# Kernel tuning notes

Hardware: AMD Instinct MI355X
Metric: run time of the kernel (lower is better)

Reference implementation:

```python
import jax, jax.numpy as jnp
import numpy as np

LEAKY_SLOPE = 0.01  # torch nn.LeakyReLU default

def leaky_relu(x):
    return jnp.where(x >= 0, x, LEAKY_SLOPE * x)

def setup_inputs() -> dict:
    key = jax.random.key(0)
    ks = jax.random.split(key, 11)
    B, F, C_IN, H, K, D = 2048, 512, 3, 64, 8, 128  # batch, features, expand, layer_conf[0], bucket_num, bucket_dim
    ASR, MM, OUT = 128, 768, 256
    proj_in = ASR + MM + F * D
    inp = {
        "stat_features": jax.random.uniform(ks[0], (B, F), dtype=jnp.float32),
        "asr_embeddings": jax.random.normal(ks[1], (B, ASR), dtype=jnp.float32),
        "mm_embeddings": jax.random.normal(ks[2], (B, MM), dtype=jnp.float32),
        "linear1_w": jax.random.normal(ks[3], (F, C_IN, H), dtype=jnp.float32) * (1.0 / np.sqrt(C_IN)),
        "linear1_b": jax.random.normal(ks[4], (F, 1, H), dtype=jnp.float32),
        "linear2_w": jax.random.normal(ks[5], (F, H, K), dtype=jnp.float32) * (1.0 / np.sqrt(H)),
        "linear2_b": jax.random.normal(ks[6], (F, 1, K), dtype=jnp.float32),
        "tau": jnp.ones((F, 1, K), dtype=jnp.float32),
        "emb": jax.random.normal(ks[7], (F, K, D), dtype=jnp.float32),
        "proj_w": jax.random.normal(ks[8], (OUT, proj_in), dtype=jnp.float32) * (1.0 / np.sqrt(proj_in)),
        "proj_b": jax.random.normal(ks[9], (OUT,), dtype=jnp.float32) * 0.01,
    }
    return inp

def reference(stat_features, asr_embeddings, mm_embeddings,
              linear1_w, linear1_b, linear2_w, linear2_b, tau, emb,
              proj_w, proj_b):
    # sanitize: NaN -> 0, negatives -> 0
    x = stat_features
    x = jnp.where(jnp.isnan(x) | (x < 0.0), 0.0, x)  # [B, F]

    # auto_dis: per-feature tiny MLP. x is expanded to 3 identical copies -> [B,F,1,3]
    # matmul with [F,3,H] == einsum over the 3 copies.
    B, F = x.shape
    x3 = jnp.broadcast_to(x[:, :, None], (B, F, 3))           # [B,F,3]
    h = jnp.einsum('bfc,fch->bfh', x3, linear1_w) + linear1_b[:, 0, :]  # [B,F,H]
    h = jnp.where(h >= 0, h, LEAKY_SLOPE * h)
    s = jnp.einsum('bfh,fhk->bfk', h, linear2_w) + linear2_b[:, 0, :]   # [B,F,K]
    s = jnp.where(s >= 0, s, LEAKY_SLOPE * s)
    s = s * tau[:, 0, :]
    p = jax.nn.softmax(s, axis=-1)                            # [B,F,K]
    y = jnp.einsum('bfk,fkd->bfd', p, emb)                    # [B,F,D]
    y = y.reshape(B, -1)                                      # [B, F*D] (fc = Identity)

    z = jnp.concatenate([asr_embeddings, mm_embeddings, y], axis=1)
    out = jax.nn.relu(z @ proj_w.T + proj_b)                  # [B, 256]
    return out
```

## Files before the change

### kernel.cpp

```cpp
#include <hip/hip_runtime.h>
#include <hip/hip_bf16.h>
#include <math.h>

#define LEAKY 0.01f
#define B_    2048
#define F_    512
#define H_    64
#define K_    8
#define D_    128
#define ASR_  128
#define MM_   768
#define OUT_  256
#define PROJ_IN 66432
#define ZK    4992
#define NSPLIT 4


typedef unsigned short u16;
typedef u16   u16x8 __attribute__((ext_vector_type(8)));
typedef short s16x8 __attribute__((ext_vector_type(8)));
typedef float f32x4 __attribute__((ext_vector_type(4)));

__device__ __forceinline__ u16 f2bf(float x) {
  unsigned int u = __float_as_uint(x);
  u += 0x7fffu + ((u >> 16) & 1u);
  return (u16)(u >> 16);
}

__device__ __forceinline__ float quad_sum(float g) {
  int a = __builtin_amdgcn_update_dpp(0, __float_as_int(g), 0xB1, 0xF, 0xF, true);
  g += __int_as_float(a);
  int b = __builtin_amdgcn_update_dpp(0, __float_as_int(g), 0x4E, 0xF, 0xF, true);
  return g + __int_as_float(b);
}

#define PRODUCER_BLOCKS (512 + 1024 + 896 + 224)

__global__ __launch_bounds__(256) void producer_kernel(
    const float* __restrict__ stat, const float* __restrict__ w1,
    const float* __restrict__ b1v, const float* __restrict__ w2,
    const float* __restrict__ b2v, const float* __restrict__ tauv,
    const float* __restrict__ pw, const float* __restrict__ emb,
    const float* __restrict__ asr, const float* __restrict__ mm,
    u16* __restrict__ A0, u16* __restrict__ Pf, u16* __restrict__ Wn) {
  __shared__ __align__(16) char smem[15616];
  const int bid = blockIdx.x;
  const int t = threadIdx.x;

  if (bid < 512) {
    const int f0 = (bid >> 3) * 8;
    const int o0 = (bid & 7) * 32;
    const int w = t >> 6, lam = t & 63;
    const int fl = lam >> 5, k = (lam >> 2) & 7, dq = lam & 3;
    const int fbase = f0 + 2 * w;
    float* sw = (float*)smem + w * 512;
    float* buf0 = sw;
    float* buf1 = sw + 256;
    const int wslot = lam ^ ((lam >> 3) & 7);
    const int xr = fl * 4 + dq;
    float4 e[8];
    {
      const float* ep = emb + ((size_t)(fbase + fl) * 8 + k) * 128 + dq * 32;
      #pragma unroll
      for (int j = 0; j < 8; ++j) e[j] = *(const float4*)(ep + j * 4);
    }
    const float* gsrc = pw + 896 + (size_t)fbase * 128
                        + (size_t)o0 * PROJ_IN + lam * 4;
    u16* wdst = Wn + (size_t)o0 * ZK + 896 + (size_t)(fbase + fl) * 8 + k;
    const float* rd0 = buf0 + fl * 128 + dq * 32;
    const float* rd1 = buf1 + fl * 128 + dq * 32;
    float4 va = *(const float4*)(gsrc);
    for (int rr = 0; rr < 16; ++rr) {
      const int r = 2 * rr;
      float4 vb = *(const float4*)(gsrc + (size_t)(r + 1) * PROJ_IN);
      *(float4*)(buf0 + wslot * 4) = va;
      {
        float g0 = 0.f, g1 = 0.f;
        #pragma unroll
        for (int j = 0; j < 8; ++j) {
          float4 p4 = *(const float4*)(rd0 + 4 * (j ^ xr));
          g0 = fmaf(e[j].x, p4.x, g0);
          g1 = fmaf(e[j].y, p4.y, g1);
          g0 = fmaf(e[j].z, p4.z, g0);
          g1 = fmaf(e[j].w, p4.w, g1);
        }
        float g = quad_sum(g0 + g1);
        if (dq == 0) wdst[(size_t)r * ZK] = f2bf(g);
      }
      if (r + 2 < 32)
        va = *(const float4*)(gsrc + (size_t)(r + 2) * PROJ_IN);
      *(float4*)(buf1 + wslot * 4) = vb;
      {
        float g0 = 0.f, g1 = 0.f;
        #pragma unroll
        for (int j = 0; j < 8; ++j) {
          float4 p4 = *(const float4*)(rd1 + 4 * (j ^ xr));
          g0 = fmaf(e[j].x, p4.x, g0);
          g1 = fmaf(e[j].y, p4.y, g1);
          g0 = fmaf(e[j].z, p4.z, g0);
          g1 = fmaf(e[j].w, p4.w, g1);
        }
        float g = quad_sum(g0 + g1);
        if (dq == 0) wdst[(size_t)(r + 1) * ZK] = f2bf(g);
      }
    }
  } else if (bid < 1536) {
    const int pb = bid - 512;
    const int f0 = (pb & 127) * 4;
    const int b0 = (pb >> 7) * 256;
    float* s_w1s = (float*)(smem);
    float* s_b1  = (float*)(smem + 1024);
    float* s_x   = (float*)(smem + 2048);
    {
      int fl = t >> 6, h = t & 63;
      const float* wf = w1 + (size_t)(f0 + fl) * 192;
      s_w1s[fl * 64 + h] = wf[h] + wf[64 + h] + wf[128 + h];
      s_b1[fl * 64 + h] = b1v[(size_t)(f0 + fl) * 64 + h];
    }
    {
      float4 sv = *(const float4*)(stat + (size_t)(b0 + t) * F_ + f0);
      float* xr_ = s_x + t * 5;
      xr_[0] = (sv.x >= 0.f) ? sv.x : 0.f;
      xr_[1] = (sv.y >= 0.f) ? sv.y : 0.f;
      xr_[2] = (sv.z >= 0.f) ? sv.z : 0.f;
      xr_[3] = (sv.w >= 0.f) ? sv.w : 0.f;
    }
    __syncthreads();

    const int w = t >> 6;
    const int wu = __builtin_amdgcn_readfirstlane(w);
    const int lane = t & 63;
    const float* w1p = s_w1s + w * 64;
    const float* b1p = s_b1 + w * 64;
    const float* w2u  = w2   + (size_t)(f0 + wu) * 512;
    const float* b2u  = b2v  + (size_t)(f0 + wu) * 8;
    const float* tauu = tauv + (size_t)(f0 + wu) * 8;
    float x[4];
    #pragma unroll
    for (int p = 0; p < 4; ++p) x[p] = s_x[(lane + 64 * p) * 5 + w];
    float acc[4][8] = {{0.f}};
    #pragma unroll 4
    for (int i = 0; i < 64; ++i) {
      float wv = w1p[i], bv = b1p[i];
      float4 wa = *(const float4*)(w2u + i * 8);
      float4 wb = *(const float4*)(w2u + i * 8 + 4);
      #pragma unroll
      for (int p = 0; p < 4; ++p) {
        float h0 = fmaf(x[p], wv, bv);
        float h = fmaf(LEAKY, fminf(h0, 0.f), fmaxf(h0, 0.f));
        acc[p][0] = fmaf(h, wa.x, acc[p][0]);
        acc[p][1] = fmaf(h, wa.y, acc[p][1]);
        acc[p][2] = fmaf(h, wa.z, acc[p][2]);
        acc[p][3] = fmaf(h, wa.w, acc[p][3]);
        acc[p][4] = fmaf(h, wb.x, acc[p][4]);
        acc[p][5] = fmaf(h, wb.y, acc[p][5]);
        acc[p][6] = fmaf(h, wb.z, acc[p][6]);
        acc[p][7] = fmaf(h, wb.w, acc[p][7]);
      }
    }
    #pragma unroll
    for (int p = 0; p < 4; ++p) {
      float s[K_];
      float m = -1e30f;
      #pragma unroll
      for (int kk = 0; kk < K_; ++kk) {
        float v = acc[p][kk] + b2u[kk];
        v = (v >= 0.f) ? v : LEAKY * v;
        v *= tauu[kk];
        s[kk] = v;
        m = fmaxf(m, v);
      }
      float sum = 0.f;
      #pragma unroll
      for (int kk = 0; kk < K_; ++kk) { s[kk] = __expf(s[kk] - m); sum += s[kk]; }
      float inv = 1.f / sum;
      u16x8 hv;
      #pragma unroll
      for (int kk = 0; kk < K_; ++kk) hv[kk] = f2bf(s[kk] * inv);
      *(u16x8*)(Pf + ((size_t)(f0 + w) * B_ + b0 + lane + 64 * p) * 8) = hv;
    }
  } else if (bid < 2432) {
    const int item = bid - 1536;
    const int cidx = item * 256 + t;
    const int r = cidx / 112, c = cidx % 112;
    float4 v0, v1;
    if (c < 16) {
      const float* s = asr + (size_t)r * ASR_ + c * 8;
      v0 = *(const float4*)(s); v1 = *(const float4*)(s + 4);
    } else {
      const float* s = mm + (size_t)r * MM_ + (c - 16) * 8;
      v0 = *(const float4*)(s); v1 = *(const float4*)(s + 4);
    }
    u16x8 hv = {f2bf(v0.x), f2bf(v0.y), f2bf(v0.z), f2bf(v0.w),
                f2bf(v1.x), f2bf(v1.y), f2bf(v1.z), f2bf(v1.w)};
    *(u16x8*)(A0 + (size_t)r * 896 + c * 8) = hv;
  } else {
    const int item = bid - 2432;
    #pragma unroll
    for (int rr = 0; rr < 4; ++rr) {
      int idx = item * 1024 + rr * 256 + t;
      int o = idx / 896, j = idx % 896;
      Wn[(size_t)o * ZK + j] = f2bf(pw[(size_t)o * PROJ_IN + j]);
    }
  }
}

#define SAS 72
__global__ __launch_bounds__(256) void gemm_kernel(
    const u16* __restrict__ A0, const u16* __restrict__ Pf,
    const u16* __restrict__ Wn, float* __restrict__ part) {
  const int bm0 = blockIdx.x * 64;
  const int bn0 = blockIdx.y * 64;
  const int kz  = blockIdx.z;
  const int it0 = kz * 20;
  const int itn = (kz == 3) ? 18 : 20;
  __shared__ u16 sA[64 * SAS];
  __shared__ u16 sB[64 * SAS];
  const int t = threadIdx.x;
  const int w = t >> 6, L = t & 63;
  const int l16 = L & 15, q8 = (L >> 4) * 8;
  const int wm = (w >> 1) * 32, wn = (w & 1) * 32;
  const int row = t >> 2, lk = t & 3;
  const int pp = t >> 5, pg = t & 31;
  f32x4 acc[2][2] = {{{0.f,0.f,0.f,0.f},{0.f,0.f,0.f,0.f}},
                     {{0.f,0.f,0.f,0.f},{0.f,0.f,0.f,0.f}}};
  u16x8 ra[2], rb[2];

#define LOAD_TILES(IT)                                                        \
  {                                                                           \
    const int k0_ = (IT) * 64;                                                \
    if (k0_ < 896) {                                                          \
      const u16* s_ = A0 + (size_t)(bm0 + row) * 896 + k0_ + lk * 8;          \
      ra[0] = *(const u16x8*)(s_);                                            \
      ra[1] = *(const u16x8*)(s_ + 32);                                       \
    } else {                                                                  \
      const int fb_ = (k0_ - 896) >> 3;                                       \
      const u16* s_ = Pf + ((size_t)(fb_ + pp) * B_ + bm0 + pg) * 8;          \
      ra[0] = *(const u16x8*)(s_);                                            \
      ra[1] = *(const u16x8*)(s_ + 256);                        \
    }                                                                         \
    const u16* sb_ = Wn + (size_t)(bn0 + row) * ZK + k0_ + lk * 8;            \
    rb[0] = *(const u16x8*)(sb_);                                             \
    rb[1] = *(const u16x8*)(sb_ + 32);                                        \
  }

#define STORE_TILES(IT)                                                       \
  {                                                                           \
    if ((IT) * 64 < 896) {                                                    \
      *(u16x8*)&sA[row * SAS + lk * 8]      = ra[0];                          \
      *(u16x8*)&sA[row * SAS + lk * 8 + 32] = ra[1];                          \
    } else {                                                                  \
      *(u16x8*)&sA[pg * SAS + pp * 8]        = ra[0];                         \
      *(u16x8*)&sA[(pg + 32) * SAS + pp * 8] = ra[1];                         \
    }                                                                         \
    *(u16x8*)&sB[row * SAS + lk * 8]      = rb[0];                            \
    *(u16x8*)&sB[row * SAS + lk * 8 + 32] = rb[1];                            \
  }

  LOAD_TILES(it0);
  for (int it = it0; it < it0 + itn; ++it) {
    __syncthreads();
    STORE_TILES(it);
    __syncthreads();
    if (it + 1 < it0 + itn) LOAD_TILES(it + 1);
    #pragma unroll
    for (int ks = 0; ks < 2; ++ks) {
      s16x8 a0 = *(const s16x8*)&sA[(wm + l16) * SAS + ks * 32 + q8];
      s16x8 a1 = *(const s16x8*)&sA[(wm + 16 + l16) * SAS + ks * 32 + q8];
      s16x8 b0 = *(const s16x8*)&sB[(wn + l16) * SAS + ks * 32 + q8];
      s16x8 b1 = *(const s16x8*)&sB[(wn + 16 + l16) * SAS + ks * 32 + q8];
      acc[0][0] = __builtin_amdgcn_mfma_f32_16x16x32_bf16(a0, b0, acc[0][0], 0, 0, 0);
      acc[0][1] = __builtin_amdgcn_mfma_f32_16x16x32_bf16(a0, b1, acc[0][1], 0, 0, 0);
      acc[1][0] = __builtin_amdgcn_mfma_f32_16x16x32_bf16(a1, b0, acc[1][0], 0, 0, 0);
      acc[1][1] = __builtin_amdgcn_mfma_f32_16x16x32_bf16(a1, b1, acc[1][1], 0, 0, 0);
    }
  }
#undef LOAD_TILES
#undef STORE_TILES

  float* dst = part + (size_t)kz * B_ * OUT_;
  #pragma unroll
  for (int mf = 0; mf < 2; ++mf) {
    const int r0 = bm0 + wm + mf * 16 + (L >> 4) * 4;
    #pragma unroll
    for (int nf = 0; nf < 2; ++nf) {
      const int col = bn0 + wn + nf * 16 + l16;
      #pragma unroll
      for (int i = 0; i < 4; ++i)
        dst[(size_t)(r0 + i) * OUT_ + col] = acc[mf][nf][i];
    }
  }
}

__global__ __launch_bounds__(256) void combine_kernel(
    const float* __restrict__ part, const float* __restrict__ pb,
    float* __restrict__ out) {
  const int idx4 = (blockIdx.x * 256 + threadIdx.x) * 4;
  const int o = idx4 & (OUT_ - 1);
  float4 bv = *(const float4*)(pb + o);
  float4 r = bv;
  #pragma unroll
  for (int kz = 0; kz < NSPLIT; ++kz) {
    float4 a = *(const float4*)(part + (size_t)kz * B_ * OUT_ + idx4);
    r.x += a.x; r.y += a.y; r.z += a.z; r.w += a.w;
  }
  r.x = r.x > 0.f ? r.x : 0.f;
  r.y = r.y > 0.f ? r.y : 0.f;
  r.z = r.z > 0.f ? r.z : 0.f;
  r.w = r.w > 0.f ? r.w : 0.f;
  *(float4*)(out + idx4) = r;
}

extern "C" void kernel_launch(void* const* d_in, const int* in_sizes, int n_in,
                              void* d_out, int out_size, void* d_ws, size_t ws_size,
                              hipStream_t stream) {
  (void)in_sizes; (void)n_in; (void)out_size; (void)ws_size;
  const float* stat = (const float*)d_in[0];
  const float* asr  = (const float*)d_in[1];
  const float* mm   = (const float*)d_in[2];
  const float* w1   = (const float*)d_in[3];
  const float* b1   = (const float*)d_in[4];
  const float* w2   = (const float*)d_in[5];
  const float* b2   = (const float*)d_in[6];
  const float* tau  = (const float*)d_in[7];
  const float* emb  = (const float*)d_in[8];
  const float* pw   = (const float*)d_in[9];
  const float* pb   = (const float*)d_in[10];
  float* out = (float*)d_out;
  char* ws = (char*)d_ws;
  u16*   A0   = (u16*)(ws);
  u16*   Pf   = (u16*)(ws + 3670016);
  u16*   Wn   = (u16*)(ws + 20447232);
  float* part = (float*)(ws + 23003136);

  producer_kernel<<<PRODUCER_BLOCKS, 256, 0, stream>>>(
      stat, w1, b1, w2, b2, tau, pw, emb, asr, mm, A0, Pf, Wn);
  gemm_kernel<<<dim3(B_ / 64, OUT_ / 64, NSPLIT), 256, 0, stream>>>(
      A0, Pf, Wn, part);
  combine_kernel<<<B_ * OUT_ / 1024, 256, 0, stream>>>(part, pb, out);
}
```

Measured before the change: 157.6 us.

## Double split-K to 8, deepen GEMM register prefetch and weight-prep load pipeline

Split-K for the projection GEMM goes from 4 to 8 slices, so each block runs 10 K-iterations and the grid has twice as many blocks for better CU occupancy. The GEMM now keeps two register stages of global loads in flight instead of one, and the weight-folding loop keeps four rows of loads outstanding instead of two. The goal is to hide global memory latency. In exchange, twice as many fp32 partials must be written and reduced, and the extra prefetch buffers raise register pressure.

```diff
diff --git a/kernel.cpp b/kernel.cpp
--- a/kernel.cpp
+++ b/kernel.cpp
@@ -13,7 +13,7 @@
 #define OUT_  256
 #define PROJ_IN 66432
 #define ZK    4992
-#define NSPLIT 4
+#define NSPLIT 8
 
 
 typedef unsigned short u16;
@@ -69,41 +69,33 @@
     u16* wdst = Wn + (size_t)o0 * ZK + 896 + (size_t)(fbase + fl) * 8 + k;
     const float* rd0 = buf0 + fl * 128 + dq * 32;
     const float* rd1 = buf1 + fl * 128 + dq * 32;
-    float4 va = *(const float4*)(gsrc);
-    for (int rr = 0; rr < 16; ++rr) {
-      const int r = 2 * rr;
-      float4 vb = *(const float4*)(gsrc + (size_t)(r + 1) * PROJ_IN);
-      *(float4*)(buf0 + wslot * 4) = va;
-      {
-        float g0 = 0.f, g1 = 0.f;
-        #pragma unroll
-        for (int j = 0; j < 8; ++j) {
-          float4 p4 = *(const float4*)(rd0 + 4 * (j ^ xr));
-          g0 = fmaf(e[j].x, p4.x, g0);
-          g1 = fmaf(e[j].y, p4.y, g1);
-          g0 = fmaf(e[j].z, p4.z, g0);
-          g1 = fmaf(e[j].w, p4.w, g1);
-        }
-        float g = quad_sum(g0 + g1);
-        if (dq == 0) wdst[(size_t)r * ZK] = f2bf(g);
-      }
-      if (r + 2 < 32)
-        va = *(const float4*)(gsrc + (size_t)(r + 2) * PROJ_IN);
-      *(float4*)(buf1 + wslot * 4) = vb;
-      {
-        float g0 = 0.f, g1 = 0.f;
-        #pragma unroll
-        for (int j = 0; j < 8; ++j) {
-          float4 p4 = *(const float4*)(rd1 + 4 * (j ^ xr));
-          g0 = fmaf(e[j].x, p4.x, g0);
-          g1 = fmaf(e[j].y, p4.y, g1);
-          g0 = fmaf(e[j].z, p4.z, g0);
-          g1 = fmaf(e[j].w, p4.w, g1);
-        }
-        float g = quad_sum(g0 + g1);
-        if (dq == 0) wdst[(size_t)(r + 1) * ZK] = f2bf(g);
-      }
-    }
+#define LDR(R) (*(const float4*)(gsrc + (size_t)(R) * PROJ_IN))
+#define WNG_ROW(BUF, RD, VREG, R, NEXT)                                       \
+    {                                                                         \
+      *(float4*)((BUF) + wslot * 4) = VREG;           \
+      if ((NEXT) < 32) VREG = LDR(NEXT);                    \
+      float g0 = 0.f, g1 = 0.f;                                               \
+      _Pragma("unroll")                                                       \
+      for (int j = 0; j < 8; ++j) {                                           \
+        float4 p4 = *(const float4*)((RD) + 4 * (j ^ xr));                    \
+        g0 = fmaf(e[j].x, p4.x, g0);                                          \
+        g1 = fmaf(e[j].y, p4.y, g1);                                          \
+        g0 = fmaf(e[j].z, p4.z, g0);                                          \
+        g1 = fmaf(e[j].w, p4.w, g1);                                          \
+      }                                                                       \
+      float g = quad_sum(g0 + g1);                                            \
+      if (dq == 0) wdst[(size_t)(R) * ZK] = f2bf(g);                          \
+    }
+    float4 va = LDR(0), vb = LDR(1), vc = LDR(2), vd = LDR(3);
+    for (int gi = 0; gi < 8; ++gi) {
+      const int r = 4 * gi;
+      WNG_ROW(buf0, rd0, va, r,     r + 4);
+      WNG_ROW(buf1, rd1, vb, r + 1, r + 5);
+      WNG_ROW(buf0, rd0, vc, r + 2, r + 6);
+      WNG_ROW(buf1, rd1, vd, r + 3, r + 7);
+    }
+#undef WNG_ROW
+#undef LDR
   } else if (bid < 1536) {
     const int pb = bid - 512;
     const int f0 = (pb & 127) * 4;
@@ -212,8 +204,8 @@
   const int bm0 = blockIdx.x * 64;
   const int bn0 = blockIdx.y * 64;
   const int kz  = blockIdx.z;
-  const int it0 = kz * 20;
-  const int itn = (kz == 3) ? 18 : 20;
+  const int it0 = kz * 10;
+  const int itn = (kz == 7) ? 8 : 10;
   __shared__ u16 sA[64 * SAS];
   __shared__ u16 sB[64 * SAS];
   const int t = threadIdx.x;
@@ -224,45 +216,47 @@
   const int pp = t >> 5, pg = t & 31;
   f32x4 acc[2][2] = {{{0.f,0.f,0.f,0.f},{0.f,0.f,0.f,0.f}},
                      {{0.f,0.f,0.f,0.f},{0.f,0.f,0.f,0.f}}};
-  u16x8 ra[2], rb[2];
-
-#define LOAD_TILES(IT)                                                        \
+  u16x8 ra[2][2], rb[2][2];
+
+#define LOAD_TILES(IT, S)                                                     \
   {                                                                           \
     const int k0_ = (IT) * 64;                                                \
     if (k0_ < 896) {                                                          \
       const u16* s_ = A0 + (size_t)(bm0 + row) * 896 + k0_ + lk * 8;          \
-      ra[0] = *(const u16x8*)(s_);                                            \
-      ra[1] = *(const u16x8*)(s_ + 32);                                       \
+      ra[S][0] = *(const u16x8*)(s_);                                         \
+      ra[S][1] = *(const u16x8*)(s_ + 32);                                    \
     } else {                                                                  \
       const int fb_ = (k0_ - 896) >> 3;                                       \
       const u16* s_ = Pf + ((size_t)(fb_ + pp) * B_ + bm0 + pg) * 8;          \
-      ra[0] = *(const u16x8*)(s_);                                            \
-      ra[1] = *(const u16x8*)(s_ + 256);                        \
+      ra[S][0] = *(const u16x8*)(s_);                                         \
+      ra[S][1] = *(const u16x8*)(s_ + 256);                     \
     }                                                                         \
     const u16* sb_ = Wn + (size_t)(bn0 + row) * ZK + k0_ + lk * 8;            \
-    rb[0] = *(const u16x8*)(sb_);                                             \
-    rb[1] = *(const u16x8*)(sb_ + 32);                                        \
-  }
-
-#define STORE_TILES(IT)                                                       \
+    rb[S][0] = *(const u16x8*)(sb_);                                          \
+    rb[S][1] = *(const u16x8*)(sb_ + 32);                                     \
+  }
+
+#define STORE_TILES(IT, S)                                                    \
   {                                                                           \
     if ((IT) * 64 < 896) {                                                    \
-      *(u16x8*)&sA[row * SAS + lk * 8]      = ra[0];                          \
-      *(u16x8*)&sA[row * SAS + lk * 8 + 32] = ra[1];                          \
+      *(u16x8*)&sA[row * SAS + lk * 8]      = ra[S][0];                       \
+      *(u16x8*)&sA[row * SAS + lk * 8 + 32] = ra[S][1];                       \
     } else {                                                                  \
-      *(u16x8*)&sA[pg * SAS + pp * 8]        = ra[0];                         \
-      *(u16x8*)&sA[(pg + 32) * SAS + pp * 8] = ra[1];                         \
+      *(u16x8*)&sA[pg * SAS + pp * 8]        = ra[S][0];                      \
+      *(u16x8*)&sA[(pg + 32) * SAS + pp * 8] = ra[S][1];                      \
     }                                                                         \
-    *(u16x8*)&sB[row * SAS + lk * 8]      = rb[0];                            \
-    *(u16x8*)&sB[row * SAS + lk * 8 + 32] = rb[1];                            \
-  }
-
-  LOAD_TILES(it0);
+    *(u16x8*)&sB[row * SAS + lk * 8]      = rb[S][0];                         \
+    *(u16x8*)&sB[row * SAS + lk * 8 + 32] = rb[S][1];                         \
+  }
+
+  LOAD_TILES(it0, 0);
+  if (itn > 1) LOAD_TILES(it0 + 1, 1);
   for (int it = it0; it < it0 + itn; ++it) {
+    const int s = it & 1;
     __syncthreads();
-    STORE_TILES(it);
+    STORE_TILES(it, s);
     __syncthreads();
-    if (it + 1 < it0 + itn) LOAD_TILES(it + 1);
+    if (it + 2 < it0 + itn) LOAD_TILES(it + 2, s);
     #pragma unroll
     for (int ks = 0; ks < 2; ++ks) {
       s16x8 a0 = *(const s16x8*)&sA[(wm + l16) * SAS + ks * 32 + q8];
```

Result: slower. 575.8 us (+265.5%).
